# Optimization experiments

Hardware: AMD Instinct MI355X
Metric: run time of the kernel (lower is better)

Reference implementation:

```python
import jax, jax.numpy as jnp
from jax import lax
import numpy as np

B = 256
EMB_DIM = 64
N_EMB = 512
LAT1 = 1024   # 16 slots * 64
LAT2 = 512
LAT = LAT1 + LAT2  # 1536
COMMIT = 0.25
EMB_COST = 1.0


def setup_inputs() -> dict:
    key = jax.random.key(0)
    ks = iter(jax.random.split(key, 40))

    def w(shape, fan_in):
        return jax.random.normal(next(ks), shape, jnp.float32) * np.float32(1.0 / np.sqrt(fan_in))

    def b(n):
        return jax.random.normal(next(ks), (n,), jnp.float32) * np.float32(0.01)

    inp = {}
    inp['x'] = jax.random.normal(next(ks), (B, 3, 64, 64), jnp.float32)
    # encoder convs, torch OIHW layout, k=4
    inp['ew0'] = w((64, 3, 4, 4), 3 * 16);   inp['eb0'] = b(64)
    inp['ew1'] = w((64, 64, 4, 4), 64 * 16); inp['eb1'] = b(64)
    inp['ew2'] = w((128, 64, 4, 4), 64 * 16); inp['eb2'] = b(128)
    inp['ew3'] = w((256, 128, 4, 4), 128 * 16); inp['eb3'] = b(256)
    # encoder fc11: 4096 -> 1024 -> 1024 -> 1536, stored (in,out)
    inp['fw0'] = w((4096, 1024), 4096); inp['fb0'] = b(1024)
    inp['fw1'] = w((1024, 1024), 1024); inp['fb1'] = b(1024)
    inp['fw2'] = w((1024, LAT), 1024);  inp['fb2'] = b(LAT)
    # VQ codebook
    inp['codebook'] = jax.random.normal(next(ks), (N_EMB, EMB_DIM), jnp.float32)
    # decoder fc3: 1536 -> 512 -> 1024 -> 4096
    inp['gw0'] = w((LAT, 512), LAT);    inp['gb0'] = b(512)
    inp['gw1'] = w((512, 1024), 512);   inp['gb1'] = b(1024)
    inp['gw2'] = w((1024, 4096), 1024); inp['gb2'] = b(4096)
    # decoder ConvTranspose2d weights, torch layout (Cin, Cout, kh, kw)
    inp['tw0'] = w((256, 128, 4, 4), 256 * 16); inp['tb0'] = b(128)
    inp['tw1'] = w((128, 64, 4, 4), 128 * 16);  inp['tb1'] = b(64)
    inp['tw2'] = w((64, 64, 4, 4), 64 * 16);    inp['tb2'] = b(64)
    inp['tw3'] = w((64, 3, 4, 4), 64 * 16);     inp['tb3'] = b(3)
    return inp


def _conv(x, w, b):
    # Conv2d k=4 s=2 p=1 -> halves H,W
    y = lax.conv_general_dilated(x, w, (2, 2), ((1, 1), (1, 1)),
                                 dimension_numbers=('NCHW', 'OIHW', 'NCHW'))
    return y + b[None, :, None, None]


def _convt(x, w, b):
    # ConvTranspose2d k=4 s=2 p=1 -> doubles H,W.
    # Equivalent to lhs_dilation=2, pad k-1-p=2, flipped kernel, swapped I/O.
    wf = jnp.flip(w, (2, 3)).transpose(1, 0, 2, 3)
    y = lax.conv_general_dilated(x, wf, (1, 1), ((2, 2), (2, 2)),
                                 lhs_dilation=(2, 2),
                                 dimension_numbers=('NCHW', 'OIHW', 'NCHW'))
    return y + b[None, :, None, None]


def _forward(x, ew0, eb0, ew1, eb1, ew2, eb2, ew3, eb3,
             fw0, fb0, fw1, fb1, fw2, fb2, codebook,
             gw0, gb0, gw1, gb1, gw2, gb2,
             tw0, tb0, tw1, tb1, tw2, tb2, tw3, tb3):
    relu = jax.nn.relu
    # --- encoder conv stack (last conv has no ReLU) ---
    h = relu(_conv(x, ew0, eb0))
    h = relu(_conv(h, ew1, eb1))
    h = relu(_conv(h, ew2, eb2))
    h = _conv(h, ew3, eb3)                      # [B,256,4,4]
    h = h.reshape(h.shape[0], -1)               # [B,4096]
    h = relu(h @ fw0 + fb0)
    h = relu(h @ fw1 + fb1)
    z = h @ fw2 + fb2                           # [B,1536]
    # --- split content / style (isVQStyle=False) ---
    z_c = z[:, :LAT1]
    z_s = z[:, LAT1:]
    # --- vector quantize z_c (16 slots of dim 64, shared codebook) ---
    flat = z_c.reshape(-1, EMB_DIM)             # [B*16, 64]
    d = (jnp.sum(flat * flat, axis=1, keepdims=True)
         + jnp.sum(codebook * codebook, axis=1)
         - 2.0 * flat @ codebook.T)             # [B*16, 512]
    idx = jnp.argmin(d, axis=1)
    quantized = codebook[idx].reshape(z_c.shape)  # [B,1024]
    sg = lax.stop_gradient
    q_latent_loss = jnp.mean((quantized - sg(z_c)) ** 2) * EMB_COST
    e_latent_loss = jnp.mean((z_c - sg(quantized)) ** 2) * COMMIT
    loss = q_latent_loss + e_latent_loss
    quantized = z_c + sg(quantized - z_c)       # straight-through
    e = jnp.concatenate([quantized, z_s], axis=-1)  # [B,1536]
    # --- decoder ---
    g = relu(e @ gw0 + gb0)
    g = relu(g @ gw1 + gb1)
    g = (g @ gw2 + gb2).reshape(-1, 256, 4, 4)
    g = relu(_convt(g, tw0, tb0))
    g = relu(_convt(g, tw1, tb1))
    g = relu(_convt(g, tw2, tb2))
    x_recon = _convt(g, tw3, tb3)               # [B,3,64,64]
    return x_recon, loss


def reference(x, ew0, eb0, ew1, eb1, ew2, eb2, ew3, eb3,
              fw0, fb0, fw1, fb1, fw2, fb2, codebook,
              gw0, gb0, gw1, gb1, gw2, gb2,
              tw0, tb0, tw1, tb1, tw2, tb2, tw3, tb3):
    return _forward(x, ew0, eb0, ew1, eb1, ew2, eb2, ew3, eb3,
                    fw0, fb0, fw1, fb1, fw2, fb2, codebook,
                    gw0, gb0, gw1, gb1, gw2, gb2,
                    tw0, tb0, tw1, tb1, tw2, tb2, tw3, tb3)
```

## Files before the change

kernel.cpp:

```cpp
#include <hip/hip_runtime.h>
#include <hip/hip_bf16.h>


#define TPB 256
typedef __attribute__((ext_vector_type(8))) short short8v;
typedef __attribute__((ext_vector_type(4))) float f32x4;
typedef unsigned int u32;
typedef unsigned short u16;

__device__ inline u16 f2bf(float x){
  union { __hip_bfloat16 b; u16 u; } cv;
  cv.b = __float2bfloat16(x);
  return cv.u;
}
__device__ inline float bf2f(u16 h){ union{u32 u;float f;}v; v.u=((u32)h)<<16; return v.f;}
__device__ inline u32 packhl(float x){ u16 h=f2bf(x); u16 l=f2bf(x-bf2f(h)); return ((u32)l<<16)|(u32)h;}

template<int NS>
__device__ inline void splitN(float x, u16 t[3]) {
  u16 h0 = f2bf(x); t[0] = h0;
  float r1 = x - bf2f(h0);
  u16 h1 = f2bf(r1); t[1] = h1;
  if (NS == 3) { float r2 = r1 - bf2f(h1); t[2] = f2bf(r2); }
}

template<int NS, int ST>
__device__ inline void stW(u32* L, int row, int oct, const u16 hs[3][8]) {
  constexpr int SWM = (ST == 64) ? 15 : 7;
  const int sw = row & SWM;
#pragma unroll
  for (int s = 0; s < NS; ++s) {
    uint4 d;
    d.x = (u32)hs[s][0] | ((u32)hs[s][1] << 16);
    d.y = (u32)hs[s][2] | ((u32)hs[s][3] << 16);
    d.z = (u32)hs[s][4] | ((u32)hs[s][5] << 16);
    d.w = (u32)hs[s][6] | ((u32)hs[s][7] << 16);
    int ch = (((s << 2) | oct) ^ sw) << 2;
    *reinterpret_cast<uint4*>(&L[row * ST + ch]) = d;
  }
}

template<int NS, int ST>
__device__ inline void stWf(u32* L, int row, int oct, const float v[8]) {
  u16 hs[3][8];
#pragma unroll
  for (int e = 0; e < 8; ++e) {
    u16 t3[3]; splitN<NS>(v[e], t3);
    hs[0][e] = t3[0]; hs[1][e] = t3[1]; if (NS == 3) hs[2][e] = t3[2];
  }
  stW<NS, ST>(L, row, oct, hs);
}

template<int ST>
__device__ inline void stWp(u32* L, int row, int oct, int s, uint4 d) {
  constexpr int SWM = (ST == 64) ? 15 : 7;
  int ch = (((s << 2) | oct) ^ (row & SWM)) << 2;
  *reinterpret_cast<uint4*>(&L[row * ST + ch]) = d;
}

template<int ST>
__device__ inline short8v rdFrag(const u32* L, int row, int c) {
  constexpr int SWM = (ST == 64) ? 15 : 7;
  int ph = (c ^ (row & SWM)) << 2;
  return *reinterpret_cast<const short8v*>(&L[row * ST + ph]);
}

__global__ __launch_bounds__(TPB) void wsplit3_k(
    const float* __restrict__ src, u16* __restrict__ dst, int n)
{
  for (int i = blockIdx.x * TPB + threadIdx.x; i < n; i += gridDim.x * TPB) {
    u16 t3[3]; splitN<3>(src[i], t3);
    dst[i] = t3[0]; dst[i + n] = t3[1]; dst[i + 2 * n] = t3[2];
  }
}
__global__ __launch_bounds__(TPB) void wprep2_k(
    const float* __restrict__ src, u16* __restrict__ dh, u16* __restrict__ dl,
    int Ci, int Co)
{
  int K4 = Ci << 2;
  int tot = 4 * Co * K4;
  for (int i = blockIdx.x * TPB + threadIdx.x; i < tot; i += gridDim.x * TPB) {
    int par = i / (Co * K4); int rem = i - par * (Co * K4);
    int co = rem / K4; int k4 = rem - co * K4;
    int ci = k4 >> 2, ay = (k4 >> 1) & 1, ax = k4 & 1;
    int py = par >> 1, px = par & 1;
    int widx = ((1 - py) << 2) + (1 - px) + (ay << 3) + (ax << 1);
    float x = src[(((size_t)ci * Co + co) << 4) + widx];
    u16 h = f2bf(x);
    dh[i] = h; dl[i] = f2bf(x - bf2f(h));
  }
}

__global__ __launch_bounds__(TPB) void x_pad_k(
    const float* __restrict__ x, float* __restrict__ xp)
{
  int idx = blockIdx.x * TPB + threadIdx.x;
  if (idx >= 3345408) return;
  int px = idx % 66; int t = idx / 66; int py = t % 66; int p = t / 66;
  float v = 0.f;
  if (py >= 1 && py <= 64 && px >= 1 && px <= 64)
    v = x[(size_t)p * 4096 + (py - 1) * 64 + (px - 1)];
  xp[idx] = v;
}
__global__ __launch_bounds__(TPB) void zb0_k(float* __restrict__ h0p)
{
  int idx = blockIdx.x * TPB + threadIdx.x;
  if (idx >= 2162688) return;
  int p = idx / 132, k = idx % 132;
  int py, px;
  if (k < 34)       { py = 0;           px = k; }
  else if (k < 68)  { py = 33;          px = k - 34; }
  else if (k < 100) { py = k - 68 + 1;  px = 0; }
  else              { py = k - 100 + 1; px = 33; }
  h0p[(size_t)p * 1156 + py * 34 + px] = 0.f;
}

template<int RM, int OUTM>
__global__ __launch_bounds__(TPB, 2) void conv_ad(
    const float* __restrict__ in, const u16* __restrict__ wsp,
    const float* __restrict__ bias, float* __restrict__ outp,
    int Ci, int Co, int Wi, int lwo, int relu, int KSPL, int PS,
    int bS, int ciS, int Mtot)
{
  constexpr int BM = RM * 64;
  __shared__ __align__(16) u32 BL[2][64 * 64];
  const int K = Ci << 4;
  const int PW = Wi + 2;
  const int Wo = Wi >> 1;
  const int tid = threadIdx.x;
  const int m0 = blockIdx.x * BM, n0 = blockIdx.y << 6;
  const int lane = tid & 63, wv = tid >> 6, r = lane & 15, g = lane >> 4;
  const int kb0 = blockIdx.z * KSPL;
  const int kbN = min(kb0 + KSPL, K);
  const int khsel = g & 1;
  const int cig = g >> 1;
  f32x4 acc[RM][4] = {};

  int base[RM];
#pragma unroll
  for (int mm = 0; mm < RM; ++mm) {
    int cell = m0 + (wv * RM + mm) * 16 + r;
    int x = cell & (Wo - 1), y = (cell >> lwo) & (Wo - 1), b = cell >> (lwo + lwo);
    base[mm] = b * bS + (2 * y + 2 * khsel) * PW + 2 * x;
  }

  auto gA = [&](int kb, float v[RM][8]) {
    if ((kb + (g << 3)) < K) {
      int cioff = ((kb >> 4) + cig) * ciS;
#pragma unroll
      for (int mm = 0; mm < RM; ++mm) {
        const float* p = in + base[mm] + cioff;
#pragma unroll
        for (int e = 0; e < 8; ++e)
          v[mm][e] = p[(e >> 2) * PW + (e & 3)];
      }
    } else {
#pragma unroll
      for (int mm = 0; mm < RM; ++mm)
#pragma unroll
        for (int e = 0; e < 8; ++e) v[mm][e] = 0.f;
    }
  };
  auto gB = [&](int kb, uint4* d) {
    int n = tid & 63, oc2 = tid >> 6;
    int k8 = kb + (oc2 << 3);
    if (k8 < K) {
      const u16* wp = wsp + (size_t)(n0 + n) * K + k8;
      d[0] = *reinterpret_cast<const uint4*>(wp);
      d[1] = *reinterpret_cast<const uint4*>(wp + PS);
      d[2] = *reinterpret_cast<const uint4*>(wp + 2 * PS);
    } else {
      d[0] = d[1] = d[2] = make_uint4(0u, 0u, 0u, 0u);
    }
  };
  auto mkfrags = [&](const float v[8], short8v f[3]) {
    u16 hs[3][8];
#pragma unroll
    for (int e = 0; e < 8; ++e) {
      u16 t3[3]; splitN<3>(v[e], t3);
      hs[0][e] = t3[0]; hs[1][e] = t3[1]; hs[2][e] = t3[2];
    }
#pragma unroll
    for (int s = 0; s < 3; ++s) {
      union { u16 u[8]; short8v sv; } cv;
#pragma unroll
      for (int e = 0; e < 8; ++e) cv.u[e] = hs[s][e];
      f[s] = cv.sv;
    }
  };

  float vA[RM][8], vA2[RM][8];
  uint4 vB[3], vB2[3];
  gA(kb0, vA); gB(kb0, vB);
  for (int kb = kb0; kb < kbN; kb += 32) {
    u32* BLc = BL[((kb - kb0) >> 5) & 1];
    {
      int n = tid & 63, oc2 = tid >> 6;
      stWp<64>(BLc, n, oc2, 0, vB[0]);
      stWp<64>(BLc, n, oc2, 1, vB[1]);
      stWp<64>(BLc, n, oc2, 2, vB[2]);
    }
    const bool more = (kb + 32) < kbN;
    if (more) { gB(kb + 32, vB2); gA(kb + 32, vA2); }
    short8v a_[RM][3];
#pragma unroll
    for (int mm = 0; mm < RM; ++mm) mkfrags(vA[mm], a_[mm]);
    __syncthreads();
#pragma unroll
    for (int ns = 0; ns < 4; ++ns) {
      short8v b_[3];
#pragma unroll
      for (int s = 0; s < 3; ++s) b_[s] = rdFrag<64>(BLc, (ns << 4) + r, (s << 2) | g);
#pragma unroll
      for (int mm = 0; mm < RM; ++mm) {
        acc[mm][ns] = __builtin_amdgcn_mfma_f32_16x16x32_bf16(a_[mm][0], b_[0], acc[mm][ns], 0, 0, 0);
        acc[mm][ns] = __builtin_amdgcn_mfma_f32_16x16x32_bf16(a_[mm][0], b_[1], acc[mm][ns], 0, 0, 0);
        acc[mm][ns] = __builtin_amdgcn_mfma_f32_16x16x32_bf16(a_[mm][1], b_[0], acc[mm][ns], 0, 0, 0);
        acc[mm][ns] = __builtin_amdgcn_mfma_f32_16x16x32_bf16(a_[mm][1], b_[1], acc[mm][ns], 0, 0, 0);
        acc[mm][ns] = __builtin_amdgcn_mfma_f32_16x16x32_bf16(a_[mm][0], b_[2], acc[mm][ns], 0, 0, 0);
        acc[mm][ns] = __builtin_amdgcn_mfma_f32_16x16x32_bf16(a_[mm][2], b_[0], acc[mm][ns], 0, 0, 0);
      }
    }
    if (more) {
#pragma unroll
      for (int mm = 0; mm < RM; ++mm)
#pragma unroll
        for (int e = 0; e < 8; ++e) vA[mm][e] = vA2[mm][e];
#pragma unroll
      for (int s = 0; s < 3; ++s) vB[s] = vB2[s];
    }
  }
#pragma unroll
  for (int mm = 0; mm < RM; ++mm)
#pragma unroll
    for (int ns = 0; ns < 4; ++ns) {
      int c0 = m0 + (wv * RM + mm) * 16 + (g << 2);
      int co = n0 + (ns << 4) + r;
      if (OUTM == 0) {
        float bv = bias[co];
        const int OPW = Wo + 2;
        const int OPHW = OPW * OPW;
#pragma unroll
        for (int q = 0; q < 4; ++q) {
          int cell = c0 + q;
          int x = cell & (Wo - 1), y = (cell >> lwo) & (Wo - 1), b = cell >> (lwo + lwo);
          float v = acc[mm][ns][q] + bv;
          if (relu) v = fmaxf(v, 0.f);
          outp[((size_t)(b * Co + co)) * OPHW + (y + 1) * OPW + (x + 1)] = v;
        }
      } else {
        float4 o;
        o.x = acc[mm][ns][0]; o.y = acc[mm][ns][1];
        o.z = acc[mm][ns][2]; o.w = acc[mm][ns][3];
        *reinterpret_cast<float4*>(
            &outp[((size_t)(blockIdx.z * Co + co)) * Mtot + c0]) = o;
      }
    }
}

__global__ __launch_bounds__(TPB) void combine_cm_k(
    const float* __restrict__ P, const float* __restrict__ bias,
    float* __restrict__ out)
{
  int idx = blockIdx.x * TPB + threadIdx.x;
  if (idx >= 5308416) return;
  int px = idx % 18; int t = idx / 18; int py = t % 18; t /= 18;
  int b = t % 256; int co = t / 256;
  float v = 0.f;
  if (py >= 1 && py <= 16 && px >= 1 && px <= 16) {
    int cell = b * 256 + (py - 1) * 16 + (px - 1);
    v = P[(size_t)co * 65536 + cell] + P[(size_t)(64 + co) * 65536 + cell] + bias[co];
    v = fmaxf(v, 0.f);
  }
  out[idx] = v;
}

__global__ __launch_bounds__(TPB) void combine_pad_k(
    const float* __restrict__ P, const float* __restrict__ bias,
    float* __restrict__ out)
{
  int idx = blockIdx.x * TPB + threadIdx.x;
  if (idx >= 3276800) return;
  int px = idx % 10; int t = idx / 10; int py = t % 10; t /= 10;
  int co = t % 128; int b = t / 128;
  float v = 0.f;
  if (py >= 1 && py <= 8 && px >= 1 && px <= 8) {
    int cell = b * 64 + (py - 1) * 8 + (px - 1);
    float s = 0.f;
#pragma unroll
    for (int z = 0; z < 4; ++z)
      s += P[((size_t)(z * 128 + co)) * 16384 + cell];
    v = fmaxf(s + bias[co], 0.f);
  }
  out[idx] = v;
}

__global__ __launch_bounds__(TPB) void conv_combine(
    const float* __restrict__ P, const float* __restrict__ bias,
    float* __restrict__ out, int Mtot, int N, int SK, int lwo, int relu)
{
  int idx = blockIdx.x * TPB + threadIdx.x;
  int mq = Mtot >> 2;
  int co = idx / mq;
  int cell0 = (idx - co * mq) << 2;
  if (co >= N) return;
  float4 s = make_float4(0.f, 0.f, 0.f, 0.f);
  for (int z = 0; z < SK; ++z) {
    const float4 pv = *reinterpret_cast<const float4*>(
        &P[((size_t)z * N + co) * Mtot + cell0]);
    s.x += pv.x; s.y += pv.y; s.z += pv.z; s.w += pv.w;
  }
  float bv = bias[co];
  s.x += bv; s.y += bv; s.z += bv; s.w += bv;
  if (relu) { s.x = fmaxf(s.x, 0.f); s.y = fmaxf(s.y, 0.f);
              s.z = fmaxf(s.z, 0.f); s.w = fmaxf(s.w, 0.f); }
  int Wo = 1 << lwo;
  int x = cell0 & (Wo - 1), y = (cell0 >> lwo) & (Wo - 1), b = cell0 >> (lwo + lwo);
  *reinterpret_cast<float4*>(&out[(((size_t)b * N + co) * Wo + y) * Wo + x]) = s;
}

template<int NS, int OUTM>
__global__ __launch_bounds__(TPB) void gemm_mf(
    const float* __restrict__ A, const float* __restrict__ W,
    const float* __restrict__ bias, void* __restrict__ outp,
    int M, int K, int N, int KSPL)
{
  constexpr int ST = (NS == 3) ? 64 : 32;
  __shared__ __align__(16) u32 L[(64 + 64) * ST];
  u32* AL = L; u32* BL = L + 64 * ST;
  const int tid = threadIdx.x;
  const int m0 = blockIdx.x << 6, n0 = blockIdx.y << 6;
  const int lane = tid & 63, wv = tid >> 6, r = lane & 15, g = lane >> 4;
  const int kb0 = blockIdx.z * KSPL;
  const int kbN = kb0 + KSPL;
  const int cl = tid & 63, oct = tid >> 6;
  f32x4 acc[4] = {};

  float vA[8], vB[8], vA2[8], vB2[8];
  auto gA = [&](int kt, float* v) {
    const float* ap = &A[(size_t)(m0 + cl) * K + kt + (oct << 3)];
    *reinterpret_cast<float4*>(&v[0]) = *reinterpret_cast<const float4*>(ap);
    *reinterpret_cast<float4*>(&v[4]) = *reinterpret_cast<const float4*>(ap + 4);
  };
  auto gB = [&](int kt, float* v) {
#pragma unroll
    for (int e = 0; e < 8; ++e)
      v[e] = W[(size_t)(kt + (oct << 3) + e) * N + n0 + cl];
  };

  gA(kb0, vA); gB(kb0, vB);
  for (int kt = kb0; kt < kbN; kt += 32) {
    const bool more = (kt + 32) < kbN;
    if (more) { gA(kt + 32, vA2); gB(kt + 32, vB2); }
    stWf<NS, ST>(AL, cl, oct, vA);
    stWf<NS, ST>(BL, cl, oct, vB);
    __syncthreads();
    short8v a_[3];
#pragma unroll
    for (int s = 0; s < NS; ++s) a_[s] = rdFrag<ST>(AL, (wv << 4) + r, (s << 2) | g);
#pragma unroll
    for (int ns = 0; ns < 4; ++ns) {
      short8v b_[3];
#pragma unroll
      for (int s = 0; s < NS; ++s) b_[s] = rdFrag<ST>(BL, (ns << 4) + r, (s << 2) | g);
      acc[ns] = __builtin_amdgcn_mfma_f32_16x16x32_bf16(a_[0], b_[0], acc[ns], 0, 0, 0);
      acc[ns] = __builtin_amdgcn_mfma_f32_16x16x32_bf16(a_[0], b_[1], acc[ns], 0, 0, 0);
      acc[ns] = __builtin_amdgcn_mfma_f32_16x16x32_bf16(a_[1], b_[0], acc[ns], 0, 0, 0);
      if (NS == 3) {
        acc[ns] = __builtin_amdgcn_mfma_f32_16x16x32_bf16(a_[1], b_[1], acc[ns], 0, 0, 0);
        acc[ns] = __builtin_amdgcn_mfma_f32_16x16x32_bf16(a_[0], b_[2], acc[ns], 0, 0, 0);
        acc[ns] = __builtin_amdgcn_mfma_f32_16x16x32_bf16(a_[2], b_[0], acc[ns], 0, 0, 0);
      }
    }
    __syncthreads();
    if (more) {
#pragma unroll
      for (int e = 0; e < 8; ++e) { vA[e] = vA2[e]; vB[e] = vB2[e]; }
    }
  }
#pragma unroll
  for (int ns = 0; ns < 4; ++ns)
#pragma unroll
    for (int q = 0; q < 4; ++q) {
      int m = m0 + (wv << 4) + (g << 2) + q;
      int n = n0 + (ns << 4) + r;
      float v = acc[ns][q];
      if (OUTM == 0) ((float*)outp)[((size_t)blockIdx.z * M + m) * N + n] = v;
      else           ((u32*)outp)[(size_t)m * N + n] = packhl(v + bias[n]);
    }
}

__global__ __launch_bounds__(TPB) void combine_k(
    const float* __restrict__ P, const float* __restrict__ bias,
    float* __restrict__ out, int MN, int N, int SK, int relu)
{
  int i4 = (blockIdx.x * TPB + threadIdx.x) << 2;
  if (i4 >= MN) return;
  float4 s = make_float4(0.f, 0.f, 0.f, 0.f);
  for (int z = 0; z < SK; ++z) {
    const float4 pv = *reinterpret_cast<const float4*>(&P[(size_t)z * MN + i4]);
    s.x += pv.x; s.y += pv.y; s.z += pv.z; s.w += pv.w;
  }
  int n = i4 % N;
  s.x += bias[n]; s.y += bias[n + 1]; s.z += bias[n + 2]; s.w += bias[n + 3];
  if (relu) { s.x = fmaxf(s.x, 0.f); s.y = fmaxf(s.y, 0.f);
              s.z = fmaxf(s.z, 0.f); s.w = fmaxf(s.w, 0.f); }
  *reinterpret_cast<float4*>(&out[i4]) = s;
}

__global__ __launch_bounds__(TPB) void combine_pk_k(
    const float* __restrict__ P, const float* __restrict__ bias,
    u32* __restrict__ out)
{
  int i4 = (blockIdx.x * TPB + threadIdx.x) << 2;
  if (i4 >= 1048576) return;
  const float4 p0 = *reinterpret_cast<const float4*>(&P[i4]);
  const float4 p1 = *reinterpret_cast<const float4*>(&P[1048576 + i4]);
  int n = i4 % 4096;
  uint4 o;
  o.x = packhl(p0.x + p1.x + bias[n]);
  o.y = packhl(p0.y + p1.y + bias[n + 1]);
  o.z = packhl(p0.z + p1.z + bias[n + 2]);
  o.w = packhl(p0.w + p1.w + bias[n + 3]);
  *reinterpret_cast<uint4*>(&out[i4]) = o;
}

template<int BM, int EMIT, int SPLITIN>
__global__ __launch_bounds__(TPB) void convt_mf2(
    const u32* __restrict__ in, const u16* __restrict__ wth,
    const u16* __restrict__ wtl, const float* __restrict__ bias,
    u32* __restrict__ outq, int Ci, int Co, int Hi, int lwi, int relu)
{
  constexpr int ST = 32, MS = BM / 64;
  constexpr int STC = BM + 4;
  constexpr int LSZ = (BM + 64) * ST;
  static_assert(32 * STC <= LSZ, "epilogue phase must fit main LDS");
  __shared__ __align__(16) u32 L[LSZ];
  u32* AL = L; u32* BL = L + BM * ST;
  const int Wi = Hi, K4 = Ci << 2;
  const int HW = Hi * Wi, HWq = HW >> 2, Wiq = Wi >> 1;
  const int par = blockIdx.z, py = par >> 1, px = par & 1;
  const int tid = threadIdx.x;
  const int m0 = blockIdx.x * BM, n0 = blockIdx.y << 6;
  const int lane = tid & 63, wv = tid >> 6, r = lane & 15, g = lane >> 4;
  f32x4 acc[MS][4] = {};

  const int cl  = (BM == 128) ? (tid & 127) : (tid & 63);
  const int oc0 = (BM == 128) ? (tid >> 7) : (tid >> 6);
  int offT[4]; u32 mskT[4];
  {
    int cell = m0 + cl;
    int X = cell & (Wi - 1), Y = (cell >> lwi) & (Wi - 1), b = cell >> (lwi + lwi);
#pragma unroll
    for (int t = 0; t < 4; ++t) {
      int ay = t >> 1, ax = t & 1;
      int gy = Y + py - ay, gx = X + px - ax;
      bool ok = (gy >= 0 && gy < Hi && gx >= 0 && gx < Wi);
      int gyc = min(max(gy, 0), Hi - 1), gxc = min(max(gx, 0), Wi - 1);
      if (SPLITIN) {
        int q = ((gyc & 1) << 1) | (gxc & 1);
        offT[t] = q * (256 * Ci * HWq) + b * Ci * HWq + (gyc >> 1) * Wiq + (gxc >> 1);
      } else {
        offT[t] = b * Ci * HW + gyc * Wi + gxc;
      }
      mskT[t] = ok ? 0xffffffffu : 0u;
    }
  }
  const int stepCi = SPLITIN ? HWq : HW;

  auto gA = [&](int kb, u32 v[][8]) {
#pragma unroll
    for (int p = 0; p < MS; ++p) {
      int oc = oc0 + (p << 1);
      int cibase = ((kb >> 2) + (oc << 1)) * stepCi;
#pragma unroll
      for (int e = 0; e < 8; ++e) {
        int t = e & 3;
        v[p][e] = in[offT[t] + cibase + ((e >> 2) ? stepCi : 0)] & mskT[t];
      }
    }
  };
  auto gB = [&](int kb, uint4* d) {
    int n = tid & 63, oc2 = tid >> 6;
    size_t base = (size_t)(par * Co + n0 + n) * K4 + kb + (oc2 << 3);
    d[0] = *reinterpret_cast<const uint4*>(wth + base);
    d[1] = *reinterpret_cast<const uint4*>(wtl + base);
  };

  u32 vA[MS][8], vA2[MS][8];
  uint4 vB[2], vB2[2];
  gA(0, vA); gB(0, vB);
  for (int kb = 0; kb < K4; kb += 32) {
    const bool more = (kb + 32) < K4;
    if (more) { gA(kb + 32, vA2); gB(kb + 32, vB2); }
#pragma unroll
    for (int p = 0; p < MS; ++p) {
      const u32* v = vA[p];
      const int sw = cl & 7;
      int oc = oc0 + (p << 1);
      uint4 dh, dl;
      dh.x = (v[0] & 0xffffu) | (v[1] << 16);  dl.x = (v[0] >> 16) | (v[1] & 0xffff0000u);
      dh.y = (v[2] & 0xffffu) | (v[3] << 16);  dl.y = (v[2] >> 16) | (v[3] & 0xffff0000u);
      dh.z = (v[4] & 0xffffu) | (v[5] << 16);  dl.z = (v[4] >> 16) | (v[5] & 0xffff0000u);
      dh.w = (v[6] & 0xffffu) | (v[7] << 16);  dl.w = (v[6] >> 16) | (v[7] & 0xffff0000u);
      *reinterpret_cast<uint4*>(&AL[cl * ST + ((oc ^ sw) << 2)]) = dh;
      *reinterpret_cast<uint4*>(&AL[cl * ST + (((4 | oc) ^ sw) << 2)]) = dl;
    }
    {
      int n = tid & 63, oc2 = tid >> 6;
      stWp<ST>(BL, n, oc2, 0, vB[0]);
      stWp<ST>(BL, n, oc2, 1, vB[1]);
    }
    __syncthreads();
    short8v a_[MS][2];
#pragma unroll
    for (int mm = 0; mm < MS; ++mm)
#pragma unroll
      for (int s = 0; s < 2; ++s)
        a_[mm][s] = rdFrag<ST>(AL, (wv * MS + mm) * 16 + r, (s << 2) | g);
#pragma unroll
    for (int ns = 0; ns < 4; ++ns) {
      short8v b_[2];
#pragma unroll
      for (int s = 0; s < 2; ++s) b_[s] = rdFrag<ST>(BL, (ns << 4) + r, (s << 2) | g);
#pragma unroll
      for (int mm = 0; mm < MS; ++mm) {
        acc[mm][ns] = __builtin_amdgcn_mfma_f32_16x16x32_bf16(a_[mm][0], b_[0], acc[mm][ns], 0, 0, 0);
        acc[mm][ns] = __builtin_amdgcn_mfma_f32_16x16x32_bf16(a_[mm][0], b_[1], acc[mm][ns], 0, 0, 0);
        acc[mm][ns] = __builtin_amdgcn_mfma_f32_16x16x32_bf16(a_[mm][1], b_[0], acc[mm][ns], 0, 0, 0);
      }
    }
    __syncthreads();
    if (more) {
#pragma unroll
      for (int p = 0; p < MS; ++p)
#pragma unroll
        for (int e = 0; e < 8; ++e) vA[p][e] = vA2[p][e];
      vB[0] = vB2[0]; vB[1] = vB2[1];
    }
  }
  const size_t QO = (size_t)256 * Co * HW;
  u32* op = outq + (size_t)par * QO;
  constexpr int C4N = BM / 4;
  constexpr int NCH = (BM * 32) / (TPB * 4);
#pragma unroll
  for (int ph = 0; ph < 2; ++ph) {
    __syncthreads();
#pragma unroll
    for (int mm = 0; mm < MS; ++mm)
#pragma unroll
      for (int nn = 0; nn < 2; ++nn) {
        int ns = (ph << 1) + nn;
#pragma unroll
        for (int q = 0; q < 4; ++q) {
          int cell = (wv * MS + mm) * 16 + (g << 2) + q;
          int colL = (nn << 4) + r;
          float v = acc[mm][ns][q] + bias[n0 + (ph << 5) + colL];
          if (relu) v = fmaxf(v, 0.f);
          L[colL * STC + cell] = EMIT ? packhl(v) : __float_as_uint(v);
        }
      }
    __syncthreads();
#pragma unroll
    for (int it = 0; it < NCH; ++it) {
      int lin = it * TPB + tid;
      int c4 = lin & (C4N - 1);
      int colL = lin / C4N;
      int col = (ph << 5) + colL;
      int cell0 = c4 << 2;
      uint4 d = *reinterpret_cast<const uint4*>(&L[colL * STC + cell0]);
      int gc = m0 + cell0;
      int Xo = gc & (Wi - 1), Yo = (gc >> lwi) & (Wi - 1), bo = gc >> (lwi + lwi);
      *reinterpret_cast<uint4*>(
          &op[((size_t)(bo * Co + n0 + col) * Hi + Yo) * Wi + Xo]) = d;
    }
  }
}

__global__ __launch_bounds__(TPB) void convt3_kernel(
    const float* __restrict__ inq, const float* __restrict__ w,
    float* __restrict__ part)
{
  __shared__ float wl[3072];
  __shared__ float il[8][33 * 32];
  const int b = blockIdx.x;
  const int z = blockIdx.y;
  const int tid = threadIdx.x;
  for (int i = tid; i < 3072; i += TPB) wl[i] = w[i];
  const int Y = tid >> 3;
  const int X0 = (tid & 7) << 2;
  float acc[3][2][8];
#pragma unroll
  for (int o = 0; o < 3; ++o)
#pragma unroll
    for (int p = 0; p < 2; ++p)
#pragma unroll
      for (int q = 0; q < 8; ++q) acc[o][p][q] = 0.f;

  const int cbeg = z << 5, cend = cbeg + 32;
  for (int c0 = cbeg; c0 < cend; c0 += 8) {
    __syncthreads();
    for (int i = tid; i < 8192; i += TPB) {
      int cc = i >> 10, yy = (i >> 5) & 31, xx = i & 31;
      int q = ((yy & 1) << 1) | (xx & 1);
      il[cc][yy * 33 + xx] = inq[(size_t)q * 4194304 +
          (((size_t)b * 64 + c0 + cc) * 16 + (yy >> 1)) * 16 + (xx >> 1)];
    }
    __syncthreads();
    for (int cc = 0; cc < 8; ++cc) {
      float iv[3][6];
#pragma unroll
      for (int j = 0; j < 3; ++j) {
        int gy = Y - 1 + j;
        int gyc = min(max(gy, 0), 31);
        float my = (gy >= 0 && gy < 32) ? 1.f : 0.f;
#pragma unroll
        for (int k = 0; k < 6; ++k) {
          int gx = X0 - 1 + k;
          int gxc = min(max(gx, 0), 31);
          float mx = (gx >= 0 && gx < 32) ? 1.f : 0.f;
          iv[j][k] = il[cc][gyc * 33 + gxc] * (my * mx);
        }
      }
      const float* wq = &wl[(c0 + cc) * 48];
#pragma unroll
      for (int o = 0; o < 3; ++o) {
        const float* wo = wq + o * 16;
#pragma unroll
        for (int c = 0; c < 4; ++c) {
          acc[o][0][2*c]   = fmaf(iv[1][c+1], wo[5],  acc[o][0][2*c]);
          acc[o][0][2*c]   = fmaf(iv[1][c],   wo[7],  acc[o][0][2*c]);
          acc[o][0][2*c]   = fmaf(iv[0][c+1], wo[13], acc[o][0][2*c]);
          acc[o][0][2*c]   = fmaf(iv[0][c],   wo[15], acc[o][0][2*c]);
          acc[o][0][2*c+1] = fmaf(iv[1][c+2], wo[4],  acc[o][0][2*c+1]);
          acc[o][0][2*c+1] = fmaf(iv[1][c+1], wo[6],  acc[o][0][2*c+1]);
          acc[o][0][2*c+1] = fmaf(iv[0][c+2], wo[12], acc[o][0][2*c+1]);
          acc[o][0][2*c+1] = fmaf(iv[0][c+1], wo[14], acc[o][0][2*c+1]);
          acc[o][1][2*c]   = fmaf(iv[2][c+1], wo[1],  acc[o][1][2*c]);
          acc[o][1][2*c]   = fmaf(iv[2][c],   wo[3],  acc[o][1][2*c]);
          acc[o][1][2*c]   = fmaf(iv[1][c+1], wo[9],  acc[o][1][2*c]);
          acc[o][1][2*c]   = fmaf(iv[1][c],   wo[11], acc[o][1][2*c]);
          acc[o][1][2*c+1] = fmaf(iv[2][c+2], wo[0],  acc[o][1][2*c+1]);
          acc[o][1][2*c+1] = fmaf(iv[2][c+1], wo[2],  acc[o][1][2*c+1]);
          acc[o][1][2*c+1] = fmaf(iv[1][c+2], wo[8],  acc[o][1][2*c+1]);
          acc[o][1][2*c+1] = fmaf(iv[1][c+1], wo[10], acc[o][1][2*c+1]);
        }
      }
    }
  }
  float* pz = part + (size_t)z * 3145728;
#pragma unroll
  for (int o = 0; o < 3; ++o) {
#pragma unroll
    for (int p = 0; p < 2; ++p) {
      float* op = pz + (((size_t)b * 3 + o) * 64 + 2 * Y + p) * 64 + 2 * X0;
      *reinterpret_cast<float4*>(op) =
          make_float4(acc[o][p][0], acc[o][p][1], acc[o][p][2], acc[o][p][3]);
      *reinterpret_cast<float4*>(op + 4) =
          make_float4(acc[o][p][4], acc[o][p][5], acc[o][p][6], acc[o][p][7]);
    }
  }
}

__global__ __launch_bounds__(TPB) void c3_combine(
    const float* __restrict__ part, const float* __restrict__ bias,
    float* __restrict__ out)
{
  int i4 = (blockIdx.x * TPB + threadIdx.x) << 2;
  const float4 p0 = *reinterpret_cast<const float4*>(&part[i4]);
  const float4 p1 = *reinterpret_cast<const float4*>(&part[i4 + 3145728]);
  int o = (i4 >> 12) % 3;
  float bv = bias[o];
  float4 s = make_float4(p0.x + p1.x + bv, p0.y + p1.y + bv,
                         p0.z + p1.z + bv, p0.w + p1.w + bv);
  *reinterpret_cast<float4*>(&out[i4]) = s;
}

__global__ __launch_bounds__(TPB) void vq8_kernel(
    const float* __restrict__ z, const float* __restrict__ cb,
    float* __restrict__ e, float* __restrict__ rowloss)
{
  __shared__ float cbL[64][65];
  __shared__ float zr[8][64];
  const int tid = threadIdx.x;
  const int lane = tid & 63, wid = tid >> 6;
  const int r0 = blockIdx.x << 3;

  for (int i = tid; i < 512; i += TPB) {
    int rr = i >> 6, k = i & 63;
    int row = r0 + rr;
    int b = row >> 4, s = row & 15;
    zr[rr][k] = z[(size_t)b * 1536 + s * 64 + k];
  }

  float best[2] = {3.4e38f, 3.4e38f};
  int bi[2] = {0, 0};

  for (int c0 = 0; c0 < 512; c0 += 64) {
    __syncthreads();
#pragma unroll
    for (int i = 0; i < 4; ++i) {
      int j = (tid >> 4) + (i << 4);
      int kq = tid & 15;
      const float4 v = *reinterpret_cast<const float4*>(
          &cb[(size_t)(c0 + j) * 64 + (kq << 2)]);
      cbL[(kq << 2) + 0][j] = v.x;
      cbL[(kq << 2) + 1][j] = v.y;
      cbL[(kq << 2) + 2][j] = v.z;
      cbL[(kq << 2) + 3][j] = v.w;
    }
    __syncthreads();
#pragma unroll
    for (int rep = 0; rep < 2; ++rep) {
      const float* zp = zr[wid + (rep << 2)];
      float d = 0.f;
#pragma unroll
      for (int k = 0; k < 64; ++k) {
        float t = zp[k] - cbL[k][lane];
        d = fmaf(t, t, d);
      }
      if (d < best[rep]) { best[rep] = d; bi[rep] = c0 + lane; }
    }
  }
#pragma unroll
  for (int rep = 0; rep < 2; ++rep) {
#pragma unroll
    for (int off = 32; off > 0; off >>= 1) {
      float ob = __shfl_xor(best[rep], off);
      int   oi = __shfl_xor(bi[rep], off);
      if (ob < best[rep] || (ob == best[rep] && oi < bi[rep])) {
        best[rep] = ob; bi[rep] = oi;
      }
    }
    int row = r0 + wid + (rep << 2);
    int b = row >> 4, s = row & 15;
    e[(size_t)b * 1536 + s * 64 + lane] = cb[(size_t)bi[rep] * 64 + lane];
    if (lane == 0) rowloss[row] = best[rep];
  }
}

__global__ __launch_bounds__(TPB) void zs_copy_kernel(
    const float* __restrict__ z, float* __restrict__ e)
{
  int i = blockIdx.x * TPB + threadIdx.x;
  int b = i >> 9, k = i & 511;
  e[(size_t)b * 1536 + 1024 + k] = z[(size_t)b * 1536 + 1024 + k];
}

__global__ __launch_bounds__(TPB) void loss_reduce_kernel(
    const float* __restrict__ rl, float* __restrict__ out)
{
  __shared__ float sm[TPB];
  float s = 0.f;
  for (int i = threadIdx.x; i < 4096; i += TPB) s += rl[i];
  sm[threadIdx.x] = s;
  __syncthreads();
  for (int sft = 128; sft > 0; sft >>= 1) {
    if (threadIdx.x < sft) sm[threadIdx.x] += sm[threadIdx.x + sft];
    __syncthreads();
  }
  if (threadIdx.x == 0) out[0] = sm[0] * (1.25f / 262144.f);
}

extern "C" void kernel_launch(void* const* d_in, const int* in_sizes, int n_in,
                              void* d_out, int out_size, void* d_ws, size_t ws_size,
                              hipStream_t stream)
{
  const float* x    = (const float*)d_in[0];
  const float* ew0  = (const float*)d_in[1];
  const float* eb0  = (const float*)d_in[2];
  const float* ew1  = (const float*)d_in[3];
  const float* eb1  = (const float*)d_in[4];
  const float* ew2  = (const float*)d_in[5];
  const float* eb2  = (const float*)d_in[6];
  const float* ew3  = (const float*)d_in[7];
  const float* eb3  = (const float*)d_in[8];
  const float* fw0  = (const float*)d_in[9];
  const float* fb0  = (const float*)d_in[10];
  const float* fw1  = (const float*)d_in[11];
  const float* fb1  = (const float*)d_in[12];
  const float* fw2  = (const float*)d_in[13];
  const float* fb2  = (const float*)d_in[14];
  const float* cb   = (const float*)d_in[15];
  const float* gw0  = (const float*)d_in[16];
  const float* gb0  = (const float*)d_in[17];
  const float* gw1  = (const float*)d_in[18];
  const float* gb1  = (const float*)d_in[19];
  const float* gw2  = (const float*)d_in[20];
  const float* gb2  = (const float*)d_in[21];
  const float* tw0  = (const float*)d_in[22];
  const float* tb0  = (const float*)d_in[23];
  const float* tw1  = (const float*)d_in[24];
  const float* tb1  = (const float*)d_in[25];
  const float* tw2  = (const float*)d_in[26];
  const float* tb2  = (const float*)d_in[27];
  const float* tw3  = (const float*)d_in[28];
  const float* tb3  = (const float*)d_in[29];

  float* out = (float*)d_out;
  float* ws  = (float*)d_ws;

  u16*   WE0  = (u16*)(ws + 0);
  u16*   WE1  = (u16*)(ws + 4608);
  u16*   WE2  = (u16*)(ws + 102912);
  u16*   WE3  = (u16*)(ws + 299520);
  float* RL   = ws + 1085952;
  float* H0P  = ws + 1090048;
  float* PC1  = ws + 20029952;
  float* XP   = ws + 20029952;
  float* H1P  = ws + 1090048;
  float* PC23 = ws + 6398464;
  float* H2P  = ws + 14787072;
  float* H3   = ws + 18063872;
  float* P    = ws + 1090048;
  float* F0   = ws + 5284352;
  float* F1   = ws + 5546496;
  float* Z    = ws + 5808640;
  float* E    = ws + 6201856;
  float* G0   = ws + 6595072;
  float* G1   = ws + 6726144;
  float* T2S  = ws + 1090048;
  u16*   WT0h = (u16*)(ws + 17867264);
  u16*   WT0l = (u16*)(ws + 18129408);
  u16*   WT1h = (u16*)(ws + 18391552);
  u16*   WT1l = (u16*)(ws + 18457088);
  u16*   WT2h = (u16*)(ws + 18522624);
  u16*   WT2l = (u16*)(ws + 18555392);
  float* PG2  = ws + 18588160;
  u32*   G2P  = (u32*)(ws + 20685312);
  u32*   T0S  = (u32*)(ws + 21733888);
  u32*   T1S  = (u32*)(ws + 23831040);
  float* PT3  = ws + 18588160;

  wsplit3_k<<<dim3(12),  TPB, 0, stream>>>(ew0, WE0, 3072);
  wsplit3_k<<<dim3(256), TPB, 0, stream>>>(ew1, WE1, 65536);
  wsplit3_k<<<dim3(512), TPB, 0, stream>>>(ew2, WE2, 131072);
  wsplit3_k<<<dim3(1024),TPB, 0, stream>>>(ew3, WE3, 524288);
  x_pad_k<<<dim3(13068), TPB, 0, stream>>>(x, XP);
  zb0_k<<<dim3(8448), TPB, 0, stream>>>(H0P);

  conv_ad<4,0><<<dim3(1024, 1, 1), TPB, 0, stream>>>(
      XP, WE0, eb0, H0P, 3, 64, 64, 5, 1, 48, 3072, 13068, 4356, 0);
  conv_ad<4,1><<<dim3(256, 1, 2), TPB, 0, stream>>>(
      H0P, WE1, eb1, PC1, 64, 64, 32, 4, 1, 512, 65536, 73984, 1156, 65536);
  combine_cm_k<<<dim3(20736), TPB, 0, stream>>>(PC1, eb1, H1P);
  conv_ad<4,1><<<dim3(64, 2, 4), TPB, 0, stream>>>(
      H1P, WE2, eb2, PC23, 64, 128, 16, 3, 1, 256, 131072, 324, 82944, 16384);
  combine_pad_k<<<dim3(12800), TPB, 0, stream>>>(PC23, eb2, H2P);
  conv_ad<4,1><<<dim3(16, 4, 8), TPB, 0, stream>>>(
      H2P, WE3, eb3, PC23, 128, 256, 8, 2, 0, 256, 524288, 12800, 100, 4096);
  conv_combine<<<dim3(1024), TPB, 0, stream>>>(PC23, eb3, H3, 4096, 256, 8, 2, 0);

  gemm_mf<3,0><<<dim3(4, 16, 16), TPB, 0, stream>>>(H3, fw0, fb0, (void*)P, 256, 4096, 1024, 256);
  combine_k<<<dim3(256), TPB, 0, stream>>>(P, fb0, F0, 262144, 1024, 16, 1);
  gemm_mf<3,0><<<dim3(4, 16, 8), TPB, 0, stream>>>(F0, fw1, fb1, (void*)P, 256, 1024, 1024, 128);
  combine_k<<<dim3(256), TPB, 0, stream>>>(P, fb1, F1, 262144, 1024, 8, 1);
  gemm_mf<3,0><<<dim3(4, 24, 8), TPB, 0, stream>>>(F1, fw2, fb2, (void*)P, 256, 1024, 1536, 128);
  combine_k<<<dim3(384), TPB, 0, stream>>>(P, fb2, Z, 393216, 1536, 8, 0);

  vq8_kernel<<<dim3(512), TPB, 0, stream>>>(Z, cb, E, RL);
  zs_copy_kernel<<<dim3(512), TPB, 0, stream>>>(Z, E);
  loss_reduce_kernel<<<dim3(1), TPB, 0, stream>>>(RL, out + (size_t)out_size - 1);

  gemm_mf<2,0><<<dim3(4, 8, 8), TPB, 0, stream>>>(E,  gw0, gb0, (void*)P, 256, 1536, 512, 192);
  combine_k<<<dim3(128), TPB, 0, stream>>>(P, gb0, G0, 131072, 512, 8, 1);
  gemm_mf<2,0><<<dim3(4, 16, 4), TPB, 0, stream>>>(G0, gw1, gb1, (void*)P, 256, 512, 1024, 128);
  combine_k<<<dim3(256), TPB, 0, stream>>>(P, gb1, G1, 262144, 1024, 4, 1);

  wprep2_k<<<dim3(512), TPB, 0, stream>>>(tw0, WT0h, WT0l, 256, 128);
  wprep2_k<<<dim3(128), TPB, 0, stream>>>(tw1, WT1h, WT1l, 128, 64);
  wprep2_k<<<dim3(64),  TPB, 0, stream>>>(tw2, WT2h, WT2l, 64, 64);

  gemm_mf<2,0><<<dim3(4, 64, 2), TPB, 0, stream>>>(G1, gw2, gb2, (void*)PG2, 256, 1024, 4096, 512);
  combine_pk_k<<<dim3(1024), TPB, 0, stream>>>(PG2, gb2, G2P);

  convt_mf2<64,1,0><<<dim3(64, 2, 4),   TPB, 0, stream>>>(G2P, WT0h, WT0l, tb0, T0S, 256, 128, 4,  2, 1);
  convt_mf2<128,1,1><<<dim3(128, 1, 4), TPB, 0, stream>>>(T0S, WT1h, WT1l, tb1, T1S, 128, 64,  8,  3, 1);
  convt_mf2<128,0,1><<<dim3(512, 1, 4), TPB, 0, stream>>>(T1S, WT2h, WT2l, tb2, (u32*)T2S, 64, 64, 16, 4, 1);
  convt3_kernel<<<dim3(256, 2), TPB, 0, stream>>>(T2S, tw3, PT3);
  c3_combine<<<dim3(3072), TPB, 0, stream>>>(PT3, tb3, out);
}
```

Measured before the change: 532.0 us.

## Load conv-transpose A fragments directly into registers and double-buffer B in LDS

The transposed-conv MFMA kernel no longer stages the im2col A operand through LDS. Each lane gathers its own A fragment from global memory straight into registers, and the weight B tile is double-buffered in LDS so the second barrier per k-step can be dropped. The M tile per block is doubled (RM×64), halving grid size, and the epilogue is done in four 16-column phases to fit the smaller LDS. The intent is to cut LDS traffic and synchronization. In exchange, A prefetch is lost (loads are no longer overlapped), register pressure rises, and there are fewer blocks.

```diff
diff --git a/kernel.cpp b/kernel.cpp
--- a/kernel.cpp
+++ b/kernel.cpp
@@ -425,31 +425,30 @@
   *reinterpret_cast<uint4*>(&out[i4]) = o;
 }
 
-template<int BM, int EMIT, int SPLITIN>
-__global__ __launch_bounds__(TPB) void convt_mf2(
+template<int RM, int EMIT, int SPLITIN>
+__global__ __launch_bounds__(TPB) void convt_ad(
     const u32* __restrict__ in, const u16* __restrict__ wth,
     const u16* __restrict__ wtl, const float* __restrict__ bias,
     u32* __restrict__ outq, int Ci, int Co, int Hi, int lwi, int relu)
 {
-  constexpr int ST = 32, MS = BM / 64;
+  constexpr int BM = RM * 64;
   constexpr int STC = BM + 4;
-  constexpr int LSZ = (BM + 64) * ST;
-  static_assert(32 * STC <= LSZ, "epilogue phase must fit main LDS");
+  constexpr int LB = 2 * 64 * 32;
+  constexpr int LSZ = (LB > 16 * STC) ? LB : 16 * STC;
   __shared__ __align__(16) u32 L[LSZ];
-  u32* AL = L; u32* BL = L + BM * ST;
   const int Wi = Hi, K4 = Ci << 2;
   const int HW = Hi * Wi, HWq = HW >> 2, Wiq = Wi >> 1;
   const int par = blockIdx.z, py = par >> 1, px = par & 1;
   const int tid = threadIdx.x;
   const int m0 = blockIdx.x * BM, n0 = blockIdx.y << 6;
   const int lane = tid & 63, wv = tid >> 6, r = lane & 15, g = lane >> 4;
-  f32x4 acc[MS][4] = {};
-
-  const int cl  = (BM == 128) ? (tid & 127) : (tid & 63);
-  const int oc0 = (BM == 128) ? (tid >> 7) : (tid >> 6);
-  int offT[4]; u32 mskT[4];
-  {
-    int cell = m0 + cl;
+  const int stepCi = SPLITIN ? HWq : HW;
+  f32x4 acc[RM][4] = {};
+
+  int offT[RM][4]; u32 mskT[RM][4];
+#pragma unroll
+  for (int mm = 0; mm < RM; ++mm) {
+    int cell = m0 + (wv * RM + mm) * 16 + r;
     int X = cell & (Wi - 1), Y = (cell >> lwi) & (Wi - 1), b = cell >> (lwi + lwi);
 #pragma unroll
     for (int t = 0; t < 4; ++t) {
@@ -459,27 +458,14 @@
       int gyc = min(max(gy, 0), Hi - 1), gxc = min(max(gx, 0), Wi - 1);
       if (SPLITIN) {
         int q = ((gyc & 1) << 1) | (gxc & 1);
-        offT[t] = q * (256 * Ci * HWq) + b * Ci * HWq + (gyc >> 1) * Wiq + (gxc >> 1);
+        offT[mm][t] = q * (256 * Ci * HWq) + b * Ci * HWq + (gyc >> 1) * Wiq + (gxc >> 1);
       } else {
-        offT[t] = b * Ci * HW + gyc * Wi + gxc;
-      }
-      mskT[t] = ok ? 0xffffffffu : 0u;
-    }
-  }
-  const int stepCi = SPLITIN ? HWq : HW;
-
-  auto gA = [&](int kb, u32 v[][8]) {
-#pragma unroll
-    for (int p = 0; p < MS; ++p) {
-      int oc = oc0 + (p << 1);
-      int cibase = ((kb >> 2) + (oc << 1)) * stepCi;
-#pragma unroll
-      for (int e = 0; e < 8; ++e) {
-        int t = e & 3;
-        v[p][e] = in[offT[t] + cibase + ((e >> 2) ? stepCi : 0)] & mskT[t];
-      }
-    }
-  };
+        offT[mm][t] = b * Ci * HW + gyc * Wi + gxc;
+      }
+      mskT[mm][t] = ok ? 0xffffffffu : 0u;
+    }
+  }
+
   auto gB = [&](int kb, uint4* d) {
     int n = tid & 63, oc2 = tid >> 6;
     size_t base = (size_t)(par * Co + n0 + n) * K4 + kb + (oc2 << 3);
@@ -487,86 +473,79 @@
     d[1] = *reinterpret_cast<const uint4*>(wtl + base);
   };
 
-  u32 vA[MS][8], vA2[MS][8];
   uint4 vB[2], vB2[2];
-  gA(0, vA); gB(0, vB);
+  gB(0, vB);
+  u32 vA[RM][8];
+  int cur = 0;
   for (int kb = 0; kb < K4; kb += 32) {
-    const bool more = (kb + 32) < K4;
-    if (more) { gA(kb + 32, vA2); gB(kb + 32, vB2); }
-#pragma unroll
-    for (int p = 0; p < MS; ++p) {
-      const u32* v = vA[p];
-      const int sw = cl & 7;
-      int oc = oc0 + (p << 1);
-      uint4 dh, dl;
-      dh.x = (v[0] & 0xffffu) | (v[1] << 16);  dl.x = (v[0] >> 16) | (v[1] & 0xffff0000u);
-      dh.y = (v[2] & 0xffffu) | (v[3] << 16);  dl.y = (v[2] >> 16) | (v[3] & 0xffff0000u);
-      dh.z = (v[4] & 0xffffu) | (v[5] << 16);  dl.z = (v[4] >> 16) | (v[5] & 0xffff0000u);
-      dh.w = (v[6] & 0xffffu) | (v[7] << 16);  dl.w = (v[6] >> 16) | (v[7] & 0xffff0000u);
-      *reinterpret_cast<uint4*>(&AL[cl * ST + ((oc ^ sw) << 2)]) = dh;
-      *reinterpret_cast<uint4*>(&AL[cl * ST + (((4 | oc) ^ sw) << 2)]) = dl;
-    }
+    {
+      int cib = ((kb >> 2) + (g << 1)) * stepCi;
+#pragma unroll
+      for (int mm = 0; mm < RM; ++mm)
+#pragma unroll
+        for (int e = 0; e < 8; ++e) {
+          int t = e & 3;
+          vA[mm][e] = in[offT[mm][t] + cib + ((e >> 2) ? stepCi : 0)] & mskT[mm][t];
+        }
+    }
+    u32* BLc = L + cur * (64 * 32);
     {
       int n = tid & 63, oc2 = tid >> 6;
-      stWp<ST>(BL, n, oc2, 0, vB[0]);
-      stWp<ST>(BL, n, oc2, 1, vB[1]);
-    }
-    __syncthreads();
-    short8v a_[MS][2];
-#pragma unroll
-    for (int mm = 0; mm < MS; ++mm)
-#pragma unroll
-      for (int s = 0; s < 2; ++s)
-        a_[mm][s] = rdFrag<ST>(AL, (wv * MS + mm) * 16 + r, (s << 2) | g);
+      stWp<32>(BLc, n, oc2, 0, vB[0]);
+      stWp<32>(BLc, n, oc2, 1, vB[1]);
+    }
+    const bool more = (kb + 32) < K4;
+    if (more) gB(kb + 32, vB2);
+    __syncthreads();
+    short8v a_[RM][2];
+#pragma unroll
+    for (int mm = 0; mm < RM; ++mm) {
+      const u32* v = vA[mm];
+      union { uint4 u; short8v s; } ch, clo;
+      ch.u.x = (v[0] & 0xffffu) | (v[1] << 16);  clo.u.x = (v[0] >> 16) | (v[1] & 0xffff0000u);
+      ch.u.y = (v[2] & 0xffffu) | (v[3] << 16);  clo.u.y = (v[2] >> 16) | (v[3] & 0xffff0000u);
+      ch.u.z = (v[4] & 0xffffu) | (v[5] << 16);  clo.u.z = (v[4] >> 16) | (v[5] & 0xffff0000u);
+      ch.u.w = (v[6] & 0xffffu) | (v[7] << 16);  clo.u.w = (v[6] >> 16) | (v[7] & 0xffff0000u);
+      a_[mm][0] = ch.s; a_[mm][1] = clo.s;
+    }
 #pragma unroll
     for (int ns = 0; ns < 4; ++ns) {
       short8v b_[2];
 #pragma unroll
-      for (int s = 0; s < 2; ++s) b_[s] = rdFrag<ST>(BL, (ns << 4) + r, (s << 2) | g);
-#pragma unroll
-      for (int mm = 0; mm < MS; ++mm) {
+      for (int s = 0; s < 2; ++s) b_[s] = rdFrag<32>(BLc, (ns << 4) + r, (s << 2) | g);
+#pragma unroll
+      for (int mm = 0; mm < RM; ++mm) {
         acc[mm][ns] = __builtin_amdgcn_mfma_f32_16x16x32_bf16(a_[mm][0], b_[0], acc[mm][ns], 0, 0, 0);
         acc[mm][ns] = __builtin_amdgcn_mfma_f32_16x16x32_bf16(a_[mm][0], b_[1], acc[mm][ns], 0, 0, 0);
         acc[mm][ns] = __builtin_amdgcn_mfma_f32_16x16x32_bf16(a_[mm][1], b_[0], acc[mm][ns], 0, 0, 0);
       }
     }
-    __syncthreads();
-    if (more) {
-#pragma unroll
-      for (int p = 0; p < MS; ++p)
-#pragma unroll
-        for (int e = 0; e < 8; ++e) vA[p][e] = vA2[p][e];
-      vB[0] = vB2[0]; vB[1] = vB2[1];
-    }
+    if (more) { vB[0] = vB2[0]; vB[1] = vB2[1]; }
+    cur ^= 1;
   }
   const size_t QO = (size_t)256 * Co * HW;
   u32* op = outq + (size_t)par * QO;
   constexpr int C4N = BM / 4;
-  constexpr int NCH = (BM * 32) / (TPB * 4);
-#pragma unroll
-  for (int ph = 0; ph < 2; ++ph) {
-    __syncthreads();
-#pragma unroll
-    for (int mm = 0; mm < MS; ++mm)
-#pragma unroll
-      for (int nn = 0; nn < 2; ++nn) {
-        int ns = (ph << 1) + nn;
-#pragma unroll
-        for (int q = 0; q < 4; ++q) {
-          int cell = (wv * MS + mm) * 16 + (g << 2) + q;
-          int colL = (nn << 4) + r;
-          float v = acc[mm][ns][q] + bias[n0 + (ph << 5) + colL];
-          if (relu) v = fmaxf(v, 0.f);
-          L[colL * STC + cell] = EMIT ? packhl(v) : __float_as_uint(v);
-        }
-      }
-    __syncthreads();
-#pragma unroll
-    for (int it = 0; it < NCH; ++it) {
+#pragma unroll
+  for (int ph = 0; ph < 4; ++ph) {
+    __syncthreads();
+    float bv = bias[n0 + (ph << 4) + r];
+#pragma unroll
+    for (int mm = 0; mm < RM; ++mm)
+#pragma unroll
+      for (int q = 0; q < 4; ++q) {
+        int cell = (wv * RM + mm) * 16 + (g << 2) + q;
+        float v = acc[mm][ph][q] + bv;
+        if (relu) v = fmaxf(v, 0.f);
+        L[r * STC + cell] = EMIT ? packhl(v) : __float_as_uint(v);
+      }
+    __syncthreads();
+#pragma unroll
+    for (int it = 0; it < RM; ++it) {
       int lin = it * TPB + tid;
       int c4 = lin & (C4N - 1);
       int colL = lin / C4N;
-      int col = (ph << 5) + colL;
+      int col = (ph << 4) + colL;
       int cell0 = c4 << 2;
       uint4 d = *reinterpret_cast<const uint4*>(&L[colL * STC + cell0]);
       int gc = m0 + cell0;
@@ -874,9 +853,9 @@
   gemm_mf<2,0><<<dim3(4, 64, 2), TPB, 0, stream>>>(G1, gw2, gb2, (void*)PG2, 256, 1024, 4096, 512);
   combine_pk_k<<<dim3(1024), TPB, 0, stream>>>(PG2, gb2, G2P);
 
-  convt_mf2<64,1,0><<<dim3(64, 2, 4),   TPB, 0, stream>>>(G2P, WT0h, WT0l, tb0, T0S, 256, 128, 4,  2, 1);
-  convt_mf2<128,1,1><<<dim3(128, 1, 4), TPB, 0, stream>>>(T0S, WT1h, WT1l, tb1, T1S, 128, 64,  8,  3, 1);
-  convt_mf2<128,0,1><<<dim3(512, 1, 4), TPB, 0, stream>>>(T1S, WT2h, WT2l, tb2, (u32*)T2S, 64, 64, 16, 4, 1);
+  convt_ad<2,1,0><<<dim3(32, 2, 4),  TPB, 0, stream>>>(G2P, WT0h, WT0l, tb0, T0S, 256, 128, 4,  2, 1);
+  convt_ad<4,1,1><<<dim3(64, 1, 4),  TPB, 0, stream>>>(T0S, WT1h, WT1l, tb1, T1S, 128, 64,  8,  3, 1);
+  convt_ad<4,0,1><<<dim3(256, 1, 4), TPB, 0, stream>>>(T1S, WT2h, WT2l, tb2, (u32*)T2S, 64, 64, 16, 4, 1);
   convt3_kernel<<<dim3(256, 2), TPB, 0, stream>>>(T2S, tw3, PT3);
   c3_combine<<<dim3(3072), TPB, 0, stream>>>(PT3, tb3, out);
 }
```

Result: no change. 536.1 us (+0.8%).
